# Performance work log

Hardware: AMD Instinct MI355X
Metric: run time of the kernel (lower is better)

## Reference

```python
import jax, jax.numpy as jnp
import numpy as np
import math

CHUNK = 256
NUM_HEADS = 4
EPS = 1e-5


def setup_inputs() -> dict:
    key = jax.random.key(0)
    ks = jax.random.split(key, 12)
    B, N, F = 4, 2048, 256
    x = jax.random.normal(ks[0], (B, N, F), dtype=jnp.float32)
    adj_matrix = jax.random.randint(ks[1], (N, N), 0, 2, dtype=jnp.int32)
    s = 1.0 / math.sqrt(F)
    Wq = jax.random.normal(ks[2], (F, F), dtype=jnp.float32) * s
    bq = jnp.zeros((F,), dtype=jnp.float32)
    Wk = jax.random.normal(ks[3], (F, F), dtype=jnp.float32) * s
    bk = jnp.zeros((F,), dtype=jnp.float32)
    Wv = jax.random.normal(ks[4], (F, F), dtype=jnp.float32) * s
    bv = jnp.zeros((F,), dtype=jnp.float32)
    Wo = jax.random.normal(ks[5], (F, F), dtype=jnp.float32) * s
    bo = jnp.zeros((F,), dtype=jnp.float32)
    gamma = jnp.ones((F,), dtype=jnp.float32)
    beta = jnp.zeros((F,), dtype=jnp.float32)
    return {"x": x, "adj_matrix": adj_matrix, "Wq": Wq, "bq": bq, "Wk": Wk,
            "bk": bk, "Wv": Wv, "bv": bv, "Wo": Wo, "bo": bo,
            "gamma": gamma, "beta": beta}


def reference(x, adj_matrix, Wq, bq, Wk, bk, Wv, bv, Wo, bo, gamma, beta):
    B, N, Fin = x.shape
    H = NUM_HEADS
    Dout = Wq.shape[0]
    Dh = Dout // H
    Nc = N // CHUNK  # number of key chunks

    # projections -> [B, H, N, Dh]
    q = (x @ Wq.T + bq).reshape(B, N, H, Dh).transpose(0, 2, 1, 3)
    k = (x @ Wk.T + bk).reshape(B, N, H, Dh).transpose(0, 2, 1, 3)
    v = (x @ Wv.T + bv).reshape(B, N, H, Dh).transpose(0, 2, 1, 3)

    # key/value chunks: [B, H, Nc, CHUNK, Dh]
    kc = k.reshape(B, H, Nc, CHUNK, Dh)
    vc = v.reshape(B, H, Nc, CHUNK, Dh)

    # scores per key chunk: [B, H, N, Nc, CHUNK]
    scores = jnp.einsum('bhnd,bhjcd->bhnjc', q, kc) / jnp.sqrt(
        jnp.asarray(Dh, dtype=q.dtype))
    scores = jnp.clip(scores, -10.0, 10.0)
    # adjacency mask, chunked along keys: [1, 1, N, Nc, CHUNK]
    mask = adj_matrix.reshape(N, Nc, CHUNK)[None, None]
    scores = jnp.where(mask == 0, jnp.asarray(-10.0, scores.dtype), scores)

    # FAITHFUL quirk: softmax is taken per key chunk (last axis only) and the
    # per-chunk contexts are SUMMED -> total attention mass per query is Nc.
    attn = jax.nn.softmax(scores, axis=-1)
    ctx = jnp.einsum('bhnjc,bhjcd->bhnd', attn, vc)  # sum over chunks j

    ctx = ctx.transpose(0, 2, 1, 3).reshape(B, N, Dout)
    out = ctx @ Wo.T + bo
    out = out + x  # residual (in_features == out_features)

    mu = jnp.mean(out, axis=-1, keepdims=True)
    var = jnp.mean(jnp.square(out - mu), axis=-1, keepdims=True)
    out = (out - mu) * jax.lax.rsqrt(var + EPS) * gamma + beta
    return out
```

## Files before the change

kernel.cpp:

```cpp
#include <hip/hip_runtime.h>
#include <math.h>

#define B_     4
#define N_     2048
#define F_     256
#define H_     4
#define DH     64
#define BN     8192
#define SP     72
#define SPO    136
#define SPW    264

#define QSCALE 0.18033688011112042f
#define CLIP   14.426950408889634f

typedef _Float16 f16;
typedef _Float16 half8  __attribute__((ext_vector_type(8)));
typedef _Float16 half4v __attribute__((ext_vector_type(4)));
typedef float    floatx4 __attribute__((ext_vector_type(4)));
typedef unsigned long long u64;

__global__ __launch_bounds__(256) void prep_kernel(
    const int* __restrict__ adj, u64* __restrict__ P,
    const float* __restrict__ x,  f16* __restrict__ xh,
    const float* __restrict__ Wq, f16* __restrict__ Wqh,
    const float* __restrict__ Wk, f16* __restrict__ Wkh,
    const float* __restrict__ Wv, f16* __restrict__ Wvh,
    const float* __restrict__ Wo, f16* __restrict__ Woh)
{
    const int bid = blockIdx.x;
    if (bid < 16384) {
        const int row   = bid >> 3;
        const int chunk = bid & 7;
        const int wave  = threadIdx.x >> 6, lane = threadIdx.x & 63;
        const int key   = chunk * 256 + wave * 64 + lane;
        u64 m = __ballot(adj[(size_t)row * N_ + key] != 0);
        if (lane == 0) P[(size_t)row * 32 + chunk * 4 + wave] = m;
        return;
    }
    const float* src; f16* dst; int base;
    if      (bid < 16448) { src = Wo; dst = Woh; base = (bid - 16384) * 1024; }
    else if (bid < 16512) { src = Wq; dst = Wqh; base = (bid - 16448) * 1024; }
    else if (bid < 16576) { src = Wk; dst = Wkh; base = (bid - 16512) * 1024; }
    else if (bid < 16640) { src = Wv; dst = Wvh; base = (bid - 16576) * 1024; }
    else                  { src = x;  dst = xh;  base = (bid - 16640) * 1024; }
    const int idx = base + threadIdx.x * 4;
    float4 v = *(const float4*)(src + idx);
    half4v h; h[0] = (f16)v.x; h[1] = (f16)v.y; h[2] = (f16)v.z; h[3] = (f16)v.w;
    *(half4v*)(dst + idx) = h;
}

__global__ __launch_bounds__(256) void proj_mfma(
    const f16* __restrict__ xh,
    const f16* __restrict__ Wqh, const f16* __restrict__ Wkh, const f16* __restrict__ Wvh,
    const float* __restrict__ bq, const float* __restrict__ bk, const float* __restrict__ bv,
    f16* __restrict__ Qh, f16* __restrict__ Kh, f16* __restrict__ Vt)
{
    const int which = blockIdx.z;
    const f16*   W    = which == 0 ? Wqh : which == 1 ? Wkh : Wvh;
    const float* bias = which == 0 ? bq  : which == 1 ? bk  : bv;

    const int r0 = blockIdx.x * 64;
    const int c0 = blockIdx.y * 128;
    const int tid  = threadIdx.x;
    const int wave = tid >> 6, lane = tid & 63;
    const int quad = lane >> 4, l16 = lane & 15;
    const int row  = tid >> 2, seg  = tid & 3;
    const int wrow = tid >> 1, whalf = (tid & 1) * 32;

    __shared__ f16 smem[(64 + 128) * SP];
    f16* xs = smem;
    f16* wt = smem + 64 * SP;

    floatx4 zz = {0.f, 0.f, 0.f, 0.f};
    floatx4 acc[8] = {zz, zz, zz, zz, zz, zz, zz, zz};

    for (int f0 = 0; f0 < F_; f0 += 64) {
        const f16* xsrc = xh + (size_t)(r0 + row) * F_ + f0 + seg * 16;
        const f16* wsrc = W  + (size_t)(c0 + wrow) * F_ + f0 + whalf;
        float4 xa0 = *(const float4*)(xsrc),      xa1 = *(const float4*)(xsrc + 8);
        float4 wa0 = *(const float4*)(wsrc),      wa1 = *(const float4*)(wsrc + 8);
        float4 wa2 = *(const float4*)(wsrc + 16), wa3 = *(const float4*)(wsrc + 24);
        __syncthreads();
        *(float4*)&xs[row * SP + seg * 16]      = xa0;
        *(float4*)&xs[row * SP + seg * 16 + 8]  = xa1;
        *(float4*)&wt[wrow * SP + whalf]        = wa0;
        *(float4*)&wt[wrow * SP + whalf + 8]    = wa1;
        *(float4*)&wt[wrow * SP + whalf + 16]   = wa2;
        *(float4*)&wt[wrow * SP + whalf + 24]   = wa3;
        __syncthreads();
        half8 a0 = *(const half8*)&xs[(wave * 16 + l16) * SP + quad * 8];
        half8 a1 = *(const half8*)&xs[(wave * 16 + l16) * SP + 32 + quad * 8];
#pragma unroll
        for (int ot = 0; ot < 8; ot++) {
            half8 b0 = *(const half8*)&wt[(ot * 16 + l16) * SP + quad * 8];
            half8 b1 = *(const half8*)&wt[(ot * 16 + l16) * SP + 32 + quad * 8];
            acc[ot] = __builtin_amdgcn_mfma_f32_16x16x32_f16(a0, b0, acc[ot], 0, 0, 0);
            acc[ot] = __builtin_amdgcn_mfma_f32_16x16x32_f16(a1, b1, acc[ot], 0, 0, 0);
        }
    }

    const int bb = r0 >> 11, nn0 = r0 & (N_ - 1);

    if (which == 2) {
#pragma unroll
        for (int ot = 0; ot < 8; ot++) {
            const int o  = c0 + ot * 16 + l16;
            const int hy = o >> 6, dh = o & 63;
            const float bv_ = bias[o];
            half4v h4;
#pragma unroll
            for (int r = 0; r < 4; r++) h4[r] = (f16)(acc[ot][r] + bv_);
            *(half4v*)(Vt + (((size_t)bb * H_ + hy) * DH + dh) * N_
                          + nn0 + wave * 16 + quad * 4) = h4;
        }
    } else {
        const float scl = (which == 0) ? QSCALE : 1.0f;
        f16* dst = which == 0 ? Qh : Kh;
        __syncthreads();
        f16* outb = smem;
#pragma unroll
        for (int ot = 0; ot < 8; ot++) {
            const float bv_ = bias[c0 + ot * 16 + l16];
#pragma unroll
            for (int r = 0; r < 4; r++)
                outb[(wave * 16 + quad * 4 + r) * SPO + ot * 16 + l16] =
                    (f16)((acc[ot][r] + bv_) * scl);
        }
        __syncthreads();
        const int colb = seg * 32;
        const int hh = (c0 + colb) >> 6, dcol = (c0 + colb) & 63;
        f16* g = dst + (((size_t)bb * H_ + hh) * N_ + nn0 + row) * DH + dcol;
#pragma unroll
        for (int k = 0; k < 4; k++)
            *(float4*)(g + k * 8) = *(const float4*)&outb[row * SPO + colb + k * 8];
    }
}

__global__ __launch_bounds__(512) void attn_mfma(
    const f16* __restrict__ Qh, const f16* __restrict__ Kh,
    const f16* __restrict__ Vt, const u64* __restrict__ Padj,
    f16* __restrict__ CTXP)
{
    const int nt = blockIdx.x & 15;
    const int sp = blockIdx.x >> 4;
    const int qb = nt * 128;
    const int h  = blockIdx.y;
    const int b  = blockIdx.z;
    const int bh = b * H_ + h;
    const int tid  = threadIdx.x;
    const int wave = tid >> 6, lane = tid & 63;
    const int quad = lane >> 4, l16 = lane & 15;
    const int qrow = tid >> 2, qseg = tid & 3;
    const int kvr  = tid >> 3, kvs  = tid & 7;

    __shared__ f16 QPs[128 * SP];
    __shared__ f16 Ks[64 * SP];
    __shared__ f16 Vs[64 * SP];

    {
        const f16* src = Qh + ((size_t)bh * N_ + qb + qrow) * DH + qseg * 16;
        *(float4*)&QPs[qrow * SP + qseg * 16]     = *(const float4*)(src);
        *(float4*)&QPs[qrow * SP + qseg * 16 + 8] = *(const float4*)(src + 8);
    }
    __syncthreads();
    const half8 qf0 = *(const half8*)&QPs[(wave * 16 + l16) * SP + quad * 8];
    const half8 qf1 = *(const half8*)&QPs[(wave * 16 + l16) * SP + 32 + quad * 8];
    f16* Ps = QPs + wave * 16 * SP;

    const int qglob = qb + wave * 16 + l16;
    const u64* arow = Padj + (size_t)qglob * 32;

    floatx4 zz = {0.f, 0.f, 0.f, 0.f};
    floatx4 ctx_tot[4] = {zz, zz, zz, zz};

    for (int ci = 0; ci < 2; ci++) {
        const int c = sp * 2 + ci;
        floatx4 ctx_ch[4] = {zz, zz, zz, zz};
        float rs_ch = 0.f;

        for (int kt = 0; kt < 4; kt++) {
            const int k0 = c * 256 + kt * 64;
            const f16* ksrc = Kh + ((size_t)bh * N_ + k0 + kvr) * DH + kvs * 8;
            const f16* vsrc = Vt + ((size_t)bh * DH + kvr) * N_ + k0 + kvs * 8;
            float4 ka = *(const float4*)(ksrc);
            float4 va = *(const float4*)(vsrc);
            __syncthreads();
            *(float4*)&Ks[kvr * SP + kvs * 8] = ka;
            *(float4*)&Vs[kvr * SP + kvs * 8] = va;
            __syncthreads();

            const u64 aw = arow[k0 >> 6];
            float rs = 0.f;
#pragma unroll
            for (int m = 0; m < 4; m++) {
                floatx4 sacc = zz;
                half8 a0 = *(const half8*)&Ks[(m * 16 + l16) * SP + quad * 8];
                half8 a1 = *(const half8*)&Ks[(m * 16 + l16) * SP + 32 + quad * 8];
                sacc = __builtin_amdgcn_mfma_f32_16x16x32_f16(a0, qf0, sacc, 0, 0, 0);
                sacc = __builtin_amdgcn_mfma_f32_16x16x32_f16(a1, qf1, sacc, 0, 0, 0);
                const unsigned int nib = (unsigned int)(aw >> (m * 16 + quad * 4)) & 0xFu;
                half4v pv;
#pragma unroll
                for (int r = 0; r < 4; r++) {
                    float sv = fminf(fmaxf(sacc[r], -CLIP), CLIP);
                    sv = ((nib >> r) & 1u) ? sv : -CLIP;
                    const float ev = __builtin_amdgcn_exp2f(sv);
                    rs += ev;
                    pv[r] = (f16)ev;
                }
                *(half4v*)&Ps[l16 * SP + m * 16 + quad * 4] = pv;
            }
            rs += __shfl_xor(rs, 16);
            rs += __shfl_xor(rs, 32);
            rs_ch += rs;

            const half8 p0 = *(const half8*)&Ps[l16 * SP + quad * 8];
            const half8 p1 = *(const half8*)&Ps[l16 * SP + 32 + quad * 8];
#pragma unroll
            for (int m = 0; m < 4; m++) {
                half8 va8 = *(const half8*)&Vs[(m * 16 + l16) * SP + quad * 8];
                half8 vb8 = *(const half8*)&Vs[(m * 16 + l16) * SP + 32 + quad * 8];
                ctx_ch[m] = __builtin_amdgcn_mfma_f32_16x16x32_f16(va8, p0, ctx_ch[m], 0, 0, 0);
                ctx_ch[m] = __builtin_amdgcn_mfma_f32_16x16x32_f16(vb8, p1, ctx_ch[m], 0, 0, 0);
            }
        }

        const float inv = 1.0f / rs_ch;
#pragma unroll
        for (int m = 0; m < 4; m++)
#pragma unroll
            for (int r = 0; r < 4; r++)
                ctx_tot[m][r] += ctx_ch[m][r] * inv;
    }

    f16* dst = CTXP + (((size_t)sp * B_ + b) * N_ + qglob) * F_ + h * DH;
#pragma unroll
    for (int m = 0; m < 4; m++) {
        half4v h4;
#pragma unroll
        for (int r = 0; r < 4; r++) h4[r] = (f16)ctx_tot[m][r];
        *(half4v*)&dst[m * 16 + quad * 4] = h4;
    }
}

__global__ __launch_bounds__(256) void out_mfma(
    const f16* __restrict__ CTXP, const float* __restrict__ x,
    const f16* __restrict__ Woh, const float* __restrict__ bo,
    const float* __restrict__ gamma, const float* __restrict__ beta,
    float* __restrict__ out)
{
    const int n0 = blockIdx.x * 16;
    const int tid  = threadIdx.x;
    const int wave = tid >> 6, lane = tid & 63;
    const int quad = lane >> 4, l16 = lane & 15;
    const int wrow = tid >> 2, wseg = tid & 3;

    __shared__ f16 cs[16 * SPW];
    __shared__ f16 wtile[256 * SP];
    __shared__ float red0[4][16], red1[4][16];

    {
        const int row = tid >> 4, c0 = (tid & 15) * 16;
        const size_t S = (size_t)BN * F_;
        const f16* p = CTXP + (size_t)(n0 + row) * F_ + c0;
#pragma unroll
        for (int g = 0; g < 2; g++) {
            half8 s0 = *(const half8*)(p + g * 8);
            half8 s1 = *(const half8*)(p + S + g * 8);
            half8 s2 = *(const half8*)(p + 2 * S + g * 8);
            half8 s3 = *(const half8*)(p + 3 * S + g * 8);
            half8 o;
#pragma unroll
            for (int e = 0; e < 8; e++)
                o[e] = (f16)(((float)s0[e] + (float)s1[e]) + ((float)s2[e] + (float)s3[e]));
            *(half8*)&cs[row * SPW + c0 + g * 8] = o;
        }
    }

    floatx4 zz = {0.f, 0.f, 0.f, 0.f};
    floatx4 acc[4] = {zz, zz, zz, zz};

#pragma unroll
    for (int f0 = 0; f0 < F_; f0 += 64) {
        __syncthreads();
#pragma unroll
        for (int rr = 0; rr < 4; rr++) {
            const int o = rr * 64 + wrow;
            const f16* src = Woh + (size_t)o * F_ + f0 + wseg * 16;
            *(float4*)&wtile[o * SP + wseg * 16]     = *(const float4*)(src);
            *(float4*)&wtile[o * SP + wseg * 16 + 8] = *(const float4*)(src + 8);
        }
        __syncthreads();
        half8 a0 = *(const half8*)&cs[l16 * SPW + f0 + quad * 8];
        half8 a1 = *(const half8*)&cs[l16 * SPW + f0 + 32 + quad * 8];
#pragma unroll
        for (int ot = 0; ot < 4; ot++) {
            const int o = wave * 64 + ot * 16 + l16;
            half8 b0 = *(const half8*)&wtile[o * SP + quad * 8];
            half8 b1 = *(const half8*)&wtile[o * SP + 32 + quad * 8];
            acc[ot] = __builtin_amdgcn_mfma_f32_16x16x32_f16(a0, b0, acc[ot], 0, 0, 0);
            acc[ot] = __builtin_amdgcn_mfma_f32_16x16x32_f16(a1, b1, acc[ot], 0, 0, 0);
        }
    }

#pragma unroll
    for (int ot = 0; ot < 4; ot++) {
        const int o = wave * 64 + ot * 16 + l16;
        const float bo_ = bo[o];
#pragma unroll
        for (int r = 0; r < 4; r++)
            acc[ot][r] += bo_ + x[(size_t)(n0 + quad * 4 + r) * F_ + o];
    }

#pragma unroll
    for (int r = 0; r < 4; r++) {
        float s = (acc[0][r] + acc[1][r]) + (acc[2][r] + acc[3][r]);
        float q = (acc[0][r] * acc[0][r] + acc[1][r] * acc[1][r]) +
                  (acc[2][r] * acc[2][r] + acc[3][r] * acc[3][r]);
        s += __shfl_xor(s, 1); q += __shfl_xor(q, 1);
        s += __shfl_xor(s, 2); q += __shfl_xor(q, 2);
        s += __shfl_xor(s, 4); q += __shfl_xor(q, 4);
        s += __shfl_xor(s, 8); q += __shfl_xor(q, 8);
        if (l16 == 0) { red0[wave][quad * 4 + r] = s; red1[wave][quad * 4 + r] = q; }
    }
    __syncthreads();

#pragma unroll
    for (int r = 0; r < 4; r++) {
        const int rr = quad * 4 + r;
        const float S  = (red0[0][rr] + red0[1][rr]) + (red0[2][rr] + red0[3][rr]);
        const float Q2 = (red1[0][rr] + red1[1][rr]) + (red1[2][rr] + red1[3][rr]);
        const float mu  = S * (1.0f / F_);
        const float var = Q2 * (1.0f / F_) - mu * mu;
        const float inv = rsqrtf(var + 1e-5f);
#pragma unroll
        for (int ot = 0; ot < 4; ot++) {
            const int o = wave * 64 + ot * 16 + l16;
            out[(size_t)(n0 + rr) * F_ + o] =
                (acc[ot][r] - mu) * inv * gamma[o] + beta[o];
        }
    }
}

extern "C" void kernel_launch(void* const* d_in, const int* in_sizes, int n_in,
                              void* d_out, int out_size, void* d_ws, size_t ws_size,
                              hipStream_t stream)
{
    const float* x     = (const float*)d_in[0];
    const int*   adj   = (const int*)  d_in[1];
    const float* Wq    = (const float*)d_in[2];
    const float* bq    = (const float*)d_in[3];
    const float* Wk    = (const float*)d_in[4];
    const float* bk    = (const float*)d_in[5];
    const float* Wv    = (const float*)d_in[6];
    const float* bv    = (const float*)d_in[7];
    const float* Wo    = (const float*)d_in[8];
    const float* bo    = (const float*)d_in[9];
    const float* gamma = (const float*)d_in[10];
    const float* beta  = (const float*)d_in[11];
    float* out = (float*)d_out;

    float* ws = (float*)d_ws;
    f16*   CTXP = (f16*)(ws);
    f16*   Qh   = (f16*)(ws + 4194304);
    f16*   Kh   = (f16*)(ws + 5242880);
    f16*   Vt   = (f16*)(ws + 6291456);
    u64*   Padj = (u64*)(ws + 7340032);
    f16*   Woh  = (f16*)(ws + 7471104);
    f16*   xh   = CTXP;
    f16*   Wqh  = (f16*)(ws + 1048576);
    f16*   Wkh  = (f16*)(ws + 1081344);
    f16*   Wvh  = (f16*)(ws + 1114112);

    hipLaunchKernelGGL(prep_kernel, dim3(18688), dim3(256), 0, stream,
                       adj, Padj, x, xh, Wq, Wqh, Wk, Wkh, Wv, Wvh, Wo, Woh);
    hipLaunchKernelGGL(proj_mfma, dim3(BN / 64, 2, 3), dim3(256), 0, stream,
                       xh, Wqh, Wkh, Wvh, bq, bk, bv, Qh, Kh, Vt);
    hipLaunchKernelGGL(attn_mfma, dim3(64, H_, B_), dim3(512), 0, stream,
                       Qh, Kh, Vt, Padj, CTXP);
    hipLaunchKernelGGL(out_mfma, dim3(BN / 16), dim3(256), 0, stream,
                       CTXP, x, Woh, bo, gamma, beta, out);
}
```

Baseline: 154.6 us.

## Process two query tiles per wave in attention and widen projection blocks

```diff
diff --git a/kernel.cpp b/kernel.cpp
--- a/kernel.cpp
+++ b/kernel.cpp
@@ -8,7 +8,7 @@
 #define DH     64
 #define BN     8192
 #define SP     72
-#define SPO    136
+#define SPO2   264
 #define SPW    264
 
 #define QSCALE 0.18033688011112042f
@@ -50,51 +50,52 @@
     *(half4v*)(dst + idx) = h;
 }
 
-__global__ __launch_bounds__(256) void proj_mfma(
+__global__ __launch_bounds__(512) void proj_mfma(
     const f16* __restrict__ xh,
     const f16* __restrict__ Wqh, const f16* __restrict__ Wkh, const f16* __restrict__ Wvh,
     const float* __restrict__ bq, const float* __restrict__ bk, const float* __restrict__ bv,
     f16* __restrict__ Qh, f16* __restrict__ Kh, f16* __restrict__ Vt)
 {
-    const int which = blockIdx.z;
+    const int which = blockIdx.y;
     const f16*   W    = which == 0 ? Wqh : which == 1 ? Wkh : Wvh;
     const float* bias = which == 0 ? bq  : which == 1 ? bk  : bv;
 
     const int r0 = blockIdx.x * 64;
-    const int c0 = blockIdx.y * 128;
     const int tid  = threadIdx.x;
     const int wave = tid >> 6, lane = tid & 63;
     const int quad = lane >> 4, l16 = lane & 15;
-    const int row  = tid >> 2, seg  = tid & 3;
-    const int wrow = tid >> 1, whalf = (tid & 1) * 32;
-
-    __shared__ f16 smem[(64 + 128) * SP];
+    const int rw = wave & 3, cw = wave >> 2;
+
+    __shared__ f16 smem[(64 + 256) * SP];
     f16* xs = smem;
     f16* wt = smem + 64 * SP;
 
     floatx4 zz = {0.f, 0.f, 0.f, 0.f};
     floatx4 acc[8] = {zz, zz, zz, zz, zz, zz, zz, zz};
 
+    const int xrow = tid >> 3, xseg = (tid & 7) * 8;
+    const int wrow = tid >> 1, wh = (tid & 1) * 32;
+
     for (int f0 = 0; f0 < F_; f0 += 64) {
-        const f16* xsrc = xh + (size_t)(r0 + row) * F_ + f0 + seg * 16;
-        const f16* wsrc = W  + (size_t)(c0 + wrow) * F_ + f0 + whalf;
-        float4 xa0 = *(const float4*)(xsrc),      xa1 = *(const float4*)(xsrc + 8);
+        const f16* xsrc = xh + (size_t)(r0 + xrow) * F_ + f0 + xseg;
+        const f16* wsrc = W  + (size_t)wrow * F_ + f0 + wh;
+        float4 xa  = *(const float4*)(xsrc);
         float4 wa0 = *(const float4*)(wsrc),      wa1 = *(const float4*)(wsrc + 8);
         float4 wa2 = *(const float4*)(wsrc + 16), wa3 = *(const float4*)(wsrc + 24);
         __syncthreads();
-        *(float4*)&xs[row * SP + seg * 16]      = xa0;
-        *(float4*)&xs[row * SP + seg * 16 + 8]  = xa1;
-        *(float4*)&wt[wrow * SP + whalf]        = wa0;
-        *(float4*)&wt[wrow * SP + whalf + 8]    = wa1;
-        *(float4*)&wt[wrow * SP + whalf + 16]   = wa2;
-        *(float4*)&wt[wrow * SP + whalf + 24]   = wa3;
-        __syncthreads();
-        half8 a0 = *(const half8*)&xs[(wave * 16 + l16) * SP + quad * 8];
-        half8 a1 = *(const half8*)&xs[(wave * 16 + l16) * SP + 32 + quad * 8];
+        *(float4*)&xs[xrow * SP + xseg]   = xa;
+        *(float4*)&wt[wrow * SP + wh]      = wa0;
+        *(float4*)&wt[wrow * SP + wh + 8]  = wa1;
+        *(float4*)&wt[wrow * SP + wh + 16] = wa2;
+        *(float4*)&wt[wrow * SP + wh + 24] = wa3;
+        __syncthreads();
+        half8 a0 = *(const half8*)&xs[(rw * 16 + l16) * SP + quad * 8];
+        half8 a1 = *(const half8*)&xs[(rw * 16 + l16) * SP + 32 + quad * 8];
 #pragma unroll
         for (int ot = 0; ot < 8; ot++) {
-            half8 b0 = *(const half8*)&wt[(ot * 16 + l16) * SP + quad * 8];
-            half8 b1 = *(const half8*)&wt[(ot * 16 + l16) * SP + 32 + quad * 8];
+            const int o = cw * 128 + ot * 16 + l16;
+            half8 b0 = *(const half8*)&wt[o * SP + quad * 8];
+            half8 b1 = *(const half8*)&wt[o * SP + 32 + quad * 8];
             acc[ot] = __builtin_amdgcn_mfma_f32_16x16x32_f16(a0, b0, acc[ot], 0, 0, 0);
             acc[ot] = __builtin_amdgcn_mfma_f32_16x16x32_f16(a1, b1, acc[ot], 0, 0, 0);
         }
@@ -105,14 +106,14 @@
     if (which == 2) {
 #pragma unroll
         for (int ot = 0; ot < 8; ot++) {
-            const int o  = c0 + ot * 16 + l16;
+            const int o  = cw * 128 + ot * 16 + l16;
             const int hy = o >> 6, dh = o & 63;
             const float bv_ = bias[o];
             half4v h4;
 #pragma unroll
             for (int r = 0; r < 4; r++) h4[r] = (f16)(acc[ot][r] + bv_);
             *(half4v*)(Vt + (((size_t)bb * H_ + hy) * DH + dh) * N_
-                          + nn0 + wave * 16 + quad * 4) = h4;
+                          + nn0 + rw * 16 + quad * 4) = h4;
         }
     } else {
         const float scl = (which == 0) ? QSCALE : 1.0f;
@@ -121,23 +122,25 @@
         f16* outb = smem;
 #pragma unroll
         for (int ot = 0; ot < 8; ot++) {
-            const float bv_ = bias[c0 + ot * 16 + l16];
+            const int o = cw * 128 + ot * 16 + l16;
+            const float bv_ = bias[o];
 #pragma unroll
             for (int r = 0; r < 4; r++)
-                outb[(wave * 16 + quad * 4 + r) * SPO + ot * 16 + l16] =
+                outb[(rw * 16 + quad * 4 + r) * SPO2 + o] =
                     (f16)((acc[ot][r] + bv_) * scl);
         }
         __syncthreads();
-        const int colb = seg * 32;
-        const int hh = (c0 + colb) >> 6, dcol = (c0 + colb) & 63;
-        f16* g = dst + (((size_t)bb * H_ + hh) * N_ + nn0 + row) * DH + dcol;
+        const int grow = tid >> 3, gseg = tid & 7;
+        const int hh = gseg >> 1, dcol = (gseg & 1) * 32;
+        f16* g = dst + (((size_t)bb * H_ + hh) * N_ + nn0 + grow) * DH + dcol;
+        const f16* s = &outb[grow * SPO2 + gseg * 32];
 #pragma unroll
         for (int k = 0; k < 4; k++)
-            *(float4*)(g + k * 8) = *(const float4*)&outb[row * SPO + colb + k * 8];
+            *(float4*)(g + k * 8) = *(const float4*)(s + k * 8);
     }
 }
 
-__global__ __launch_bounds__(512) void attn_mfma(
+__global__ __launch_bounds__(256) void attn_mfma(
     const f16* __restrict__ Qh, const f16* __restrict__ Kh,
     const f16* __restrict__ Vt, const u64* __restrict__ Padj,
     f16* __restrict__ CTXP)
@@ -151,96 +154,119 @@
     const int tid  = threadIdx.x;
     const int wave = tid >> 6, lane = tid & 63;
     const int quad = lane >> 4, l16 = lane & 15;
-    const int qrow = tid >> 2, qseg = tid & 3;
-    const int kvr  = tid >> 3, kvs  = tid & 7;
 
     __shared__ f16 QPs[128 * SP];
     __shared__ f16 Ks[64 * SP];
     __shared__ f16 Vs[64 * SP];
 
     {
-        const f16* src = Qh + ((size_t)bh * N_ + qb + qrow) * DH + qseg * 16;
-        *(float4*)&QPs[qrow * SP + qseg * 16]     = *(const float4*)(src);
-        *(float4*)&QPs[qrow * SP + qseg * 16 + 8] = *(const float4*)(src + 8);
+        const int qrow = tid >> 1, qhalf = (tid & 1) * 32;
+        const f16* src = Qh + ((size_t)bh * N_ + qb + qrow) * DH + qhalf;
+#pragma unroll
+        for (int k = 0; k < 4; k++)
+            *(float4*)&QPs[qrow * SP + qhalf + k * 8] = *(const float4*)(src + k * 8);
     }
     __syncthreads();
-    const half8 qf0 = *(const half8*)&QPs[(wave * 16 + l16) * SP + quad * 8];
-    const half8 qf1 = *(const half8*)&QPs[(wave * 16 + l16) * SP + 32 + quad * 8];
-    f16* Ps = QPs + wave * 16 * SP;
-
-    const int qglob = qb + wave * 16 + l16;
-    const u64* arow = Padj + (size_t)qglob * 32;
+    const half8 qf0a = *(const half8*)&QPs[(wave * 32 + l16) * SP + quad * 8];
+    const half8 qf1a = *(const half8*)&QPs[(wave * 32 + l16) * SP + 32 + quad * 8];
+    const half8 qf0b = *(const half8*)&QPs[(wave * 32 + 16 + l16) * SP + quad * 8];
+    const half8 qf1b = *(const half8*)&QPs[(wave * 32 + 16 + l16) * SP + 32 + quad * 8];
+    f16* Ps = QPs + wave * 32 * SP;
+
+    const int qgA = qb + wave * 32 + l16;
+    const int qgB = qgA + 16;
+    const u64* arowA = Padj + (size_t)qgA * 32;
+    const u64* arowB = Padj + (size_t)qgB * 32;
 
     floatx4 zz = {0.f, 0.f, 0.f, 0.f};
-    floatx4 ctx_tot[4] = {zz, zz, zz, zz};
+    floatx4 totA[4] = {zz, zz, zz, zz}, totB[4] = {zz, zz, zz, zz};
+
+    const int kvr = tid >> 2, kvs = (tid & 3) * 16;
 
     for (int ci = 0; ci < 2; ci++) {
         const int c = sp * 2 + ci;
-        floatx4 ctx_ch[4] = {zz, zz, zz, zz};
-        float rs_ch = 0.f;
+        floatx4 chA[4] = {zz, zz, zz, zz}, chB[4] = {zz, zz, zz, zz};
+        float rsA = 0.f, rsB = 0.f;
 
         for (int kt = 0; kt < 4; kt++) {
             const int k0 = c * 256 + kt * 64;
-            const f16* ksrc = Kh + ((size_t)bh * N_ + k0 + kvr) * DH + kvs * 8;
-            const f16* vsrc = Vt + ((size_t)bh * DH + kvr) * N_ + k0 + kvs * 8;
-            float4 ka = *(const float4*)(ksrc);
-            float4 va = *(const float4*)(vsrc);
+            const f16* ksrc = Kh + ((size_t)bh * N_ + k0 + kvr) * DH + kvs;
+            const f16* vsrc = Vt + ((size_t)bh * DH + kvr) * N_ + k0 + kvs;
+            float4 ka0 = *(const float4*)(ksrc), ka1 = *(const float4*)(ksrc + 8);
+            float4 va0 = *(const float4*)(vsrc), va1 = *(const float4*)(vsrc + 8);
             __syncthreads();
-            *(float4*)&Ks[kvr * SP + kvs * 8] = ka;
-            *(float4*)&Vs[kvr * SP + kvs * 8] = va;
+            *(float4*)&Ks[kvr * SP + kvs]     = ka0;
+            *(float4*)&Ks[kvr * SP + kvs + 8] = ka1;
+            *(float4*)&Vs[kvr * SP + kvs]     = va0;
+            *(float4*)&Vs[kvr * SP + kvs + 8] = va1;
             __syncthreads();
 
-            const u64 aw = arow[k0 >> 6];
-            float rs = 0.f;
+            const u64 awA = arowA[k0 >> 6];
+            const u64 awB = arowB[k0 >> 6];
+            float rA = 0.f, rB = 0.f;
 #pragma unroll
             for (int m = 0; m < 4; m++) {
-                floatx4 sacc = zz;
                 half8 a0 = *(const half8*)&Ks[(m * 16 + l16) * SP + quad * 8];
                 half8 a1 = *(const half8*)&Ks[(m * 16 + l16) * SP + 32 + quad * 8];
-                sacc = __builtin_amdgcn_mfma_f32_16x16x32_f16(a0, qf0, sacc, 0, 0, 0);
-                sacc = __builtin_amdgcn_mfma_f32_16x16x32_f16(a1, qf1, sacc, 0, 0, 0);
-                const unsigned int nib = (unsigned int)(aw >> (m * 16 + quad * 4)) & 0xFu;
-                half4v pv;
+                floatx4 sA = zz, sB = zz;
+                sA = __builtin_amdgcn_mfma_f32_16x16x32_f16(a0, qf0a, sA, 0, 0, 0);
+                sA = __builtin_amdgcn_mfma_f32_16x16x32_f16(a1, qf1a, sA, 0, 0, 0);
+                sB = __builtin_amdgcn_mfma_f32_16x16x32_f16(a0, qf0b, sB, 0, 0, 0);
+                sB = __builtin_amdgcn_mfma_f32_16x16x32_f16(a1, qf1b, sB, 0, 0, 0);
+                const unsigned int nibA = (unsigned int)(awA >> (m * 16 + quad * 4)) & 0xFu;
+                const unsigned int nibB = (unsigned int)(awB >> (m * 16 + quad * 4)) & 0xFu;
+                half4v pA, pB;
 #pragma unroll
                 for (int r = 0; r < 4; r++) {
-                    float sv = fminf(fmaxf(sacc[r], -CLIP), CLIP);
-                    sv = ((nib >> r) & 1u) ? sv : -CLIP;
-                    const float ev = __builtin_amdgcn_exp2f(sv);
-                    rs += ev;
-                    pv[r] = (f16)ev;
+                    float svA = fminf(fmaxf(sA[r], -CLIP), CLIP);
+                    svA = ((nibA >> r) & 1u) ? svA : -CLIP;
+                    const float eA = __builtin_amdgcn_exp2f(svA);
+                    rA += eA; pA[r] = (f16)eA;
+                    float svB = fminf(fmaxf(sB[r], -CLIP), CLIP);
+                    svB = ((nibB >> r) & 1u) ? svB : -CLIP;
+                    const float eB = __builtin_amdgcn_exp2f(svB);
+                    rB += eB; pB[r] = (f16)eB;
                 }
-                *(half4v*)&Ps[l16 * SP + m * 16 + quad * 4] = pv;
+                *(half4v*)&Ps[l16 * SP + m * 16 + quad * 4]        = pA;
+                *(half4v*)&Ps[(16 + l16) * SP + m * 16 + quad * 4] = pB;
             }
-            rs += __shfl_xor(rs, 16);
-            rs += __shfl_xor(rs, 32);
-            rs_ch += rs;
-
-            const half8 p0 = *(const half8*)&Ps[l16 * SP + quad * 8];
-            const half8 p1 = *(const half8*)&Ps[l16 * SP + 32 + quad * 8];
+            rA += __shfl_xor(rA, 16); rA += __shfl_xor(rA, 32); rsA += rA;
+            rB += __shfl_xor(rB, 16); rB += __shfl_xor(rB, 32); rsB += rB;
+
+            const half8 pA0 = *(const half8*)&Ps[l16 * SP + quad * 8];
+            const half8 pA1 = *(const half8*)&Ps[l16 * SP + 32 + quad * 8];
+            const half8 pB0 = *(const half8*)&Ps[(16 + l16) * SP + quad * 8];
+            const half8 pB1 = *(const half8*)&Ps[(16 + l16) * SP + 32 + quad * 8];
 #pragma unroll
             for (int m = 0; m < 4; m++) {
                 half8 va8 = *(const half8*)&Vs[(m * 16 + l16) * SP + quad * 8];
                 half8 vb8 = *(const half8*)&Vs[(m * 16 + l16) * SP + 32 + quad * 8];
-                ctx_ch[m] = __builtin_amdgcn_mfma_f32_16x16x32_f16(va8, p0, ctx_ch[m], 0, 0, 0);
-                ctx_ch[m] = __builtin_amdgcn_mfma_f32_16x16x32_f16(vb8, p1, ctx_ch[m], 0, 0, 0);
+                chA[m] = __builtin_amdgcn_mfma_f32_16x16x32_f16(va8, pA0, chA[m], 0, 0, 0);
+                chA[m] = __builtin_amdgcn_mfma_f32_16x16x32_f16(vb8, pA1, chA[m], 0, 0, 0);
+                chB[m] = __builtin_amdgcn_mfma_f32_16x16x32_f16(va8, pB0, chB[m], 0, 0, 0);
+                chB[m] = __builtin_amdgcn_mfma_f32_16x16x32_f16(vb8, pB1, chB[m], 0, 0, 0);
             }
         }
 
-        const float inv = 1.0f / rs_ch;
+        const float invA = 1.0f / rsA, invB = 1.0f / rsB;
 #pragma unroll
         for (int m = 0; m < 4; m++)
 #pragma unroll
-            for (int r = 0; r < 4; r++)
-                ctx_tot[m][r] += ctx_ch[m][r] * inv;
-    }
-
-    f16* dst = CTXP + (((size_t)sp * B_ + b) * N_ + qglob) * F_ + h * DH;
+            for (int r = 0; r < 4; r++) {
+                totA[m][r] += chA[m][r] * invA;
+                totB[m][r] += chB[m][r] * invB;
+            }
+    }
+
+    f16* dstA = CTXP + (((size_t)sp * B_ + b) * N_ + qgA) * F_ + h * DH;
+    f16* dstB = CTXP + (((size_t)sp * B_ + b) * N_ + qgB) * F_ + h * DH;
 #pragma unroll
     for (int m = 0; m < 4; m++) {
-        half4v h4;
-#pragma unroll
-        for (int r = 0; r < 4; r++) h4[r] = (f16)ctx_tot[m][r];
-        *(half4v*)&dst[m * 16 + quad * 4] = h4;
+        half4v hA, hB;
+#pragma unroll
+        for (int r = 0; r < 4; r++) { hA[r] = (f16)totA[m][r]; hB[r] = (f16)totB[m][r]; }
+        *(half4v*)&dstA[m * 16 + quad * 4] = hA;
+        *(half4v*)&dstB[m * 16 + quad * 4] = hB;
     }
 }
 
@@ -375,9 +401,9 @@
 
     hipLaunchKernelGGL(prep_kernel, dim3(18688), dim3(256), 0, stream,
                        adj, Padj, x, xh, Wq, Wqh, Wk, Wkh, Wv, Wvh, Wo, Woh);
-    hipLaunchKernelGGL(proj_mfma, dim3(BN / 64, 2, 3), dim3(256), 0, stream,
+    hipLaunchKernelGGL(proj_mfma, dim3(BN / 64, 3), dim3(512), 0, stream,
                        xh, Wqh, Wkh, Wvh, bq, bk, bv, Qh, Kh, Vt);
-    hipLaunchKernelGGL(attn_mfma, dim3(64, H_, B_), dim3(512), 0, stream,
+    hipLaunchKernelGGL(attn_mfma, dim3(64, H_, B_), dim3(256), 0, stream,
                        Qh, Kh, Vt, Padj, CTXP);
     hipLaunchKernelGGL(out_mfma, dim3(BN / 16), dim3(256), 0, stream,
                        CTXP, x, Woh, bo, gamma, beta, out);
```

Measured after the change: 163.4 us. +5.7%, slower.
